# Optimization experiments

Hardware: AMD Instinct MI355X
Metric: run time of the kernel (lower is better)

The kernel has to match this reference:

```python
import jax, jax.numpy as jnp
import numpy as np

CAPACITY_FACTOR = 1.25


def setup_inputs() -> dict:
    key = jax.random.key(0)
    k1, k2, k3, k4, k5, k6 = jax.random.split(key, 6)
    N, d, E, h = 8192, 1024, 8, 2816
    x = jax.random.normal(k1, (N, d), dtype=jnp.float32)
    topK_indices = jax.random.randint(k2, (N,), 0, E, dtype=jnp.int64)
    topK_scores = jax.random.uniform(k3, (N,), dtype=jnp.float32)
    Wg = jax.random.normal(k4, (E, d, h), dtype=jnp.float32) * 0.02
    Wu = jax.random.normal(k5, (E, d, h), dtype=jnp.float32) * 0.02
    Wd = jax.random.normal(k6, (E, h, d), dtype=jnp.float32) * 0.02
    return {"x": x, "topK_indices": topK_indices, "topK_scores": topK_scores,
            "Wg": Wg, "Wu": Wu, "Wd": Wd}


def reference(x, topK_indices, topK_scores, Wg, Wu, Wd):
    # x: [N, d] tokens; topK_indices: [N] top-1 expert ids; per-expert SwiGLU FFN.
    N, d = x.shape
    E = Wg.shape[0]
    capacity = int(CAPACITY_FACTOR * N / E)  # = 1280

    idx = topK_indices.astype(jnp.int32)
    onehot = jax.nn.one_hot(idx, E, dtype=jnp.int32)            # [N, E]
    # position of each token within its expert's queue (first-come-first-served)
    pos = jnp.sum((jnp.cumsum(onehot, axis=0) - 1) * onehot, axis=1)  # [N]
    kept = pos < capacity                                        # dropped tokens pass through

    # flat dispatch slot: expert*capacity + pos for kept tokens, overflow bucket otherwise
    slots = jnp.where(kept, idx * capacity + pos, E * capacity)  # [N]
    buf = jnp.zeros((E * capacity + 1, d), dtype=x.dtype).at[slots].set(x)
    xe = buf[: E * capacity].reshape(E, capacity, d)             # [E, C, d]

    # per-expert SwiGLU FFN (grouped GEMMs)
    hgate = jnp.einsum('ecd,edh->ech', xe, Wg)
    hup = jnp.einsum('ecd,edh->ech', xe, Wu)
    hact = jax.nn.silu(hgate) * hup
    out = jnp.einsum('ech,ehd->ecd', hact, Wd).reshape(E * capacity, d)
    out = jnp.concatenate([out, jnp.zeros((1, d), out.dtype)], axis=0)

    y_tok = out[slots]                                           # gather back per token
    # multiply_gate_scores=True: scale expert output by routing score; dropped -> identity
    y = jnp.where(kept[:, None], y_tok * topK_scores[:, None], x)
    return y
```

## Files before the change

kernel.cpp:

```cpp
#include <hip/hip_runtime.h>
#include <cstdint>
#include <cstddef>

#define N_TOK 8192
#define DIM   1024
#define NEXP  8
#define HID   2816
#define CAP   1280

typedef __bf16 bf16x8 __attribute__((ext_vector_type(8)));
typedef float  floatx4 __attribute__((ext_vector_type(4)));

__device__ __forceinline__ unsigned short f2bf(float f) {
  return __builtin_bit_cast(unsigned short, (__bf16)f);
}
__device__ __forceinline__ float bf2f(unsigned short u) {
  return (float)__builtin_bit_cast(__bf16, u);
}

__device__ __forceinline__ void async16(void* lds, const void* g) {
  __builtin_amdgcn_global_load_lds(
      (const __attribute__((address_space(1))) void*)g,
      (__attribute__((address_space(3))) void*)lds, 16, 0, 0);
}

__global__ void route_kernel(const int* __restrict__ idx, int idx_stride,
                             int* __restrict__ slot,
                             int* __restrict__ slot_token,
                             int* __restrict__ counts) {
  __shared__ int hist[256][NEXP];
  const int t = threadIdx.x;
  int loc[NEXP];
#pragma unroll
  for (int e = 0; e < NEXP; e++) loc[e] = 0;
  const int base = t * 32;
  for (int i = 0; i < 32; i++) {
    int e = idx[(base + i) * idx_stride];
    loc[e]++;
  }
#pragma unroll
  for (int e = 0; e < NEXP; e++) hist[t][e] = loc[e];
  __syncthreads();
  if (t < NEXP) {
    int run = 0;
    for (int i = 0; i < 256; i++) { int v = hist[i][t]; hist[i][t] = run; run += v; }
    counts[t] = run < CAP ? run : CAP;
  }
  __syncthreads();
  int b2[NEXP];
#pragma unroll
  for (int e = 0; e < NEXP; e++) b2[e] = hist[t][e];
  for (int i = 0; i < 32; i++) {
    const int n = base + i;
    const int e = idx[n * idx_stride];
    const int p = b2[e]++;
    if (p < CAP) {
      const int s = e * CAP + p;
      slot[n] = s;
      slot_token[s] = n;
    } else {
      slot[n] = -1;
    }
  }
}

__global__ void dispatch_kernel(const float* __restrict__ x,
                                const int* __restrict__ slot,
                                unsigned short* __restrict__ xe,
                                float* __restrict__ y) {
  const int n = blockIdx.x;
  const int t = threadIdx.x;
  const int s = slot[n];
  const float4 v = ((const float4*)(x + (size_t)n * DIM))[t];
  if (s >= 0) {
    ushort4 b;
    b.x = f2bf(v.x); b.y = f2bf(v.y); b.z = f2bf(v.z); b.w = f2bf(v.w);
    ((ushort4*)(xe + (size_t)s * DIM))[t] = b;
  } else {
    ((float4*)(y + (size_t)n * DIM))[t] = v;
  }
}

__global__ void transpose_cvt(const float* __restrict__ in,
                              unsigned short* __restrict__ out,
                              const int R, const int C) {
  __shared__ float tile[32][33];
  const int e = blockIdx.z;
  const float* ib = in + (size_t)e * R * C;
  unsigned short* ob = out + (size_t)e * R * C;
  const int tx = threadIdx.x, ty = threadIdx.y;
  const int c0 = blockIdx.x * 32, r0 = blockIdx.y * 32;
#pragma unroll
  for (int i = 0; i < 4; i++)
    tile[ty + i * 8][tx] = ib[(size_t)(r0 + ty + i * 8) * C + c0 + tx];
  __syncthreads();
#pragma unroll
  for (int i = 0; i < 4; i++)
    ob[(size_t)(c0 + ty + i * 8) * R + r0 + tx] = f2bf(tile[tx][ty + i * 8]);
}

template <int EPI>
__global__ __launch_bounds__(256)
void moe_gemm(const unsigned short* __restrict__ A,
              const unsigned short* __restrict__ Bt,
              const int* __restrict__ counts,
              const int K, const int N,
              const size_t a_es, const size_t b_es,
              unsigned short* __restrict__ obuf,
              const int* __restrict__ slot_token,
              const float* __restrict__ scores,
              float* __restrict__ y) {
  const int e = blockIdx.z;
  const int cnt = counts[e];
  const int m0 = blockIdx.y * 128;
  if (m0 >= cnt) return;
  const int n0 = blockIdx.x * 128;

  __shared__ char smem[16384];

  const int t = threadIdx.x;
  const int lane = t & 63;
  const int w = t >> 6;
  const int wr = w >> 1;
  const int wc = w & 1;

  const unsigned short* aP  = A + e * a_es + (size_t)(m0 + (t >> 2)) * K + (t & 3) * 8;
  const unsigned short* bP  = Bt + e * b_es + (size_t)(n0 + (t >> 2)) * K + (t & 3) * 8;
  const unsigned short* aP1 = aP + (size_t)64 * K;
  const unsigned short* bP1 = bP + (size_t)64 * K;
  char* lA0 = smem + t * 16;
  char* lA1 = smem + 4096 + t * 16;
  char* lB0 = smem + 8192 + t * 16;
  char* lB1 = smem + 12288 + t * 16;

  floatx4 acc[4][4] = {};

  const int mrow = wr * 64 + (lane & 15);
  const int ncol = wc * 64 + (lane & 15);
  const int kq = (lane >> 4) * 16;

  for (int kk = 0; kk < K; kk += 32) {
    async16(lA0, aP); async16(lA1, aP1);
    async16(lB0, bP); async16(lB1, bP1);
    aP += 32; aP1 += 32; bP += 32; bP1 += 32;
    __syncthreads();
    bf16x8 af[4], bfr[4];
#pragma unroll
    for (int i = 0; i < 4; i++)
      af[i] = *(const bf16x8*)(smem + (mrow + i * 16) * 64 + kq);
#pragma unroll
    for (int i = 0; i < 4; i++)
      bfr[i] = *(const bf16x8*)(smem + 8192 + (ncol + i * 16) * 64 + kq);
#pragma unroll
    for (int mi = 0; mi < 4; mi++)
#pragma unroll
      for (int ni = 0; ni < 4; ni++)
        acc[mi][ni] = __builtin_amdgcn_mfma_f32_16x16x32_bf16(
            af[mi], bfr[ni], acc[mi][ni], 0, 0, 0);
    __syncthreads();
  }

  const int quad = lane >> 4;
  const int cl = lane & 15;

  if (EPI == 0) {
    unsigned short* ob = obuf + (size_t)e * CAP * N;
#pragma unroll
    for (int mi = 0; mi < 4; mi++)
#pragma unroll
      for (int r = 0; r < 4; r++) {
        const int row = m0 + wr * 64 + mi * 16 + quad * 4 + r;
        const size_t rb = (size_t)row * N;
#pragma unroll
        for (int ni = 0; ni < 4; ni++) {
          const int col = n0 + wc * 64 + ni * 16 + cl;
          ob[rb + col] = f2bf(acc[mi][ni][r]);
        }
      }
  } else if (EPI == 1) {
    unsigned short* ob = obuf + (size_t)e * CAP * N;
#pragma unroll
    for (int mi = 0; mi < 4; mi++)
#pragma unroll
      for (int r = 0; r < 4; r++) {
        const int row = m0 + wr * 64 + mi * 16 + quad * 4 + r;
        const size_t rb = (size_t)row * N;
#pragma unroll
        for (int ni = 0; ni < 4; ni++) {
          const int col = n0 + wc * 64 + ni * 16 + cl;
          const float g = bf2f(ob[rb + col]);
          const float u = acc[mi][ni][r];
          const float act = g / (1.0f + __expf(-g)) * u;
          ob[rb + col] = f2bf(act);
        }
      }
  } else {
#pragma unroll
    for (int mi = 0; mi < 4; mi++)
#pragma unroll
      for (int r = 0; r < 4; r++) {
        const int row = m0 + wr * 64 + mi * 16 + quad * 4 + r;
        if (row < cnt) {
          const int tok = slot_token[e * CAP + row];
          const float s = scores[tok];
          float* yr = y + (size_t)tok * DIM;
#pragma unroll
          for (int ni = 0; ni < 4; ni++) {
            const int col = n0 + wc * 64 + ni * 16 + cl;
            yr[col] = acc[mi][ni][r] * s;
          }
        }
      }
  }
}

extern "C" void kernel_launch(void* const* d_in, const int* in_sizes, int n_in,
                              void* d_out, int out_size, void* d_ws, size_t ws_size,
                              hipStream_t stream) {
  const float* x      = (const float*)d_in[0];
  const int*   idx    = (const int*)d_in[1];
  const float* scores = (const float*)d_in[2];
  const float* Wg     = (const float*)d_in[3];
  const float* Wu     = (const float*)d_in[4];
  const float* Wd     = (const float*)d_in[5];
  float* y = (float*)d_out;

  const int idx_stride = (in_sizes[1] == 2 * N_TOK) ? 2 : 1;

  char* ws = (char*)d_ws;
  size_t off = 0;
  auto alloc = [&](size_t b) -> char* {
    char* p = ws + off;
    off += (b + 255) & ~(size_t)255;
    return p;
  };
  int* counts            = (int*)alloc(NEXP * 4);
  int* slot              = (int*)alloc((size_t)N_TOK * 4);
  int* slot_token        = (int*)alloc((size_t)NEXP * CAP * 4);
  unsigned short* xe     = (unsigned short*)alloc((size_t)NEXP * CAP * DIM * 2);
  unsigned short* hbuf   = (unsigned short*)alloc((size_t)NEXP * CAP * HID * 2);
  unsigned short* wg_t   = (unsigned short*)alloc((size_t)NEXP * DIM * HID * 2);
  unsigned short* wu_t   = (unsigned short*)alloc((size_t)NEXP * DIM * HID * 2);
  unsigned short* wd_t   = (unsigned short*)alloc((size_t)NEXP * DIM * HID * 2);
  (void)ws_size; (void)n_in; (void)out_size;

  route_kernel<<<1, 256, 0, stream>>>(idx, idx_stride, slot, slot_token, counts);
  dispatch_kernel<<<N_TOK, 256, 0, stream>>>(x, slot, xe, y);

  dim3 tb(32, 8);
  transpose_cvt<<<dim3(HID / 32, DIM / 32, NEXP), tb, 0, stream>>>(Wg, wg_t, DIM, HID);
  transpose_cvt<<<dim3(HID / 32, DIM / 32, NEXP), tb, 0, stream>>>(Wu, wu_t, DIM, HID);
  transpose_cvt<<<dim3(DIM / 32, HID / 32, NEXP), tb, 0, stream>>>(Wd, wd_t, HID, DIM);

  moe_gemm<0><<<dim3(HID / 128, CAP / 128, NEXP), 256, 0, stream>>>(
      xe, wg_t, counts, DIM, HID, (size_t)CAP * DIM, (size_t)DIM * HID,
      hbuf, nullptr, nullptr, nullptr);
  moe_gemm<1><<<dim3(HID / 128, CAP / 128, NEXP), 256, 0, stream>>>(
      xe, wu_t, counts, DIM, HID, (size_t)CAP * DIM, (size_t)DIM * HID,
      hbuf, nullptr, nullptr, nullptr);
  moe_gemm<2><<<dim3(DIM / 128, CAP / 128, NEXP), 256, 0, stream>>>(
      hbuf, wd_t, counts, HID, DIM, (size_t)CAP * HID, (size_t)HID * DIM,
      nullptr, slot_token, scores, y);
}
```

Measured before the change: 645.0 us.

## Fuse gate/up GEMMs with SiLU epilogue, swizzle LDS, remap blocks per XCD

Gate and up projections now run in one kernel that shares the A tile and computes SiLU·up in registers. This removes the bf16 round trip of the gate output through global memory and one full pass over xe. LDS reads are XOR-swizzled to reduce bank conflicts. Blocks are remapped so each XCD works on contiguous expert/column groups, which should improve L2 reuse. The weight transpose uses 64x64 tiles with vectorized float4 loads and 16-byte stores.

```diff
diff --git a/kernel.cpp b/kernel.cpp
--- a/kernel.cpp
+++ b/kernel.cpp
@@ -10,12 +10,10 @@
 
 typedef __bf16 bf16x8 __attribute__((ext_vector_type(8)));
 typedef float  floatx4 __attribute__((ext_vector_type(4)));
+typedef unsigned short u16x8 __attribute__((ext_vector_type(8)));
 
 __device__ __forceinline__ unsigned short f2bf(float f) {
   return __builtin_bit_cast(unsigned short, (__bf16)f);
-}
-__device__ __forceinline__ float bf2f(unsigned short u) {
-  return (float)__builtin_bit_cast(__bf16, u);
 }
 
 __device__ __forceinline__ void async16(void* lds, const void* g) {
@@ -81,40 +79,58 @@
   }
 }
 
-__global__ void transpose_cvt(const float* __restrict__ in,
-                              unsigned short* __restrict__ out,
-                              const int R, const int C) {
-  __shared__ float tile[32][33];
+__global__ __launch_bounds__(256)
+void transpose_cvt(const float* __restrict__ in,
+                   unsigned short* __restrict__ out,
+                   const int R, const int C) {
+  __shared__ float tile[64][65];
   const int e = blockIdx.z;
   const float* ib = in + (size_t)e * R * C;
   unsigned short* ob = out + (size_t)e * R * C;
-  const int tx = threadIdx.x, ty = threadIdx.y;
-  const int c0 = blockIdx.x * 32, r0 = blockIdx.y * 32;
-#pragma unroll
-  for (int i = 0; i < 4; i++)
-    tile[ty + i * 8][tx] = ib[(size_t)(r0 + ty + i * 8) * C + c0 + tx];
+  const int t = threadIdx.x;
+  const int c0 = blockIdx.x * 64, r0 = blockIdx.y * 64;
+  const int lr = t >> 4;
+  const int lc = (t & 15) * 4;
+#pragma unroll
+  for (int i = 0; i < 4; i++) {
+    const float4 v = *(const float4*)(ib + (size_t)(r0 + lr + i * 16) * C + c0 + lc);
+    tile[lr + i * 16][lc + 0] = v.x;
+    tile[lr + i * 16][lc + 1] = v.y;
+    tile[lr + i * 16][lc + 2] = v.z;
+    tile[lr + i * 16][lc + 3] = v.w;
+  }
   __syncthreads();
-#pragma unroll
-  for (int i = 0; i < 4; i++)
-    ob[(size_t)(c0 + ty + i * 8) * R + r0 + tx] = f2bf(tile[tx][ty + i * 8]);
-}
-
-template <int EPI>
+  const int oc = t >> 2;
+  const int sub = t & 3;
+#pragma unroll
+  for (int half = 0; half < 2; half++) {
+    const int rch = sub + half * 4;
+    u16x8 o;
+#pragma unroll
+    for (int j = 0; j < 8; j++) o[j] = f2bf(tile[rch * 8 + j][oc]);
+    *(u16x8*)(ob + (size_t)(c0 + oc) * R + r0 + rch * 8) = o;
+  }
+}
+
 __global__ __launch_bounds__(256)
-void moe_gemm(const unsigned short* __restrict__ A,
-              const unsigned short* __restrict__ Bt,
-              const int* __restrict__ counts,
-              const int K, const int N,
-              const size_t a_es, const size_t b_es,
-              unsigned short* __restrict__ obuf,
-              const int* __restrict__ slot_token,
-              const float* __restrict__ scores,
-              float* __restrict__ y) {
-  const int e = blockIdx.z;
+void gateup_gemm(const unsigned short* __restrict__ A,
+                 const unsigned short* __restrict__ Bg,
+                 const unsigned short* __restrict__ Bu,
+                 const int* __restrict__ counts,
+                 unsigned short* __restrict__ hact) {
+  const int bid = blockIdx.x;
+  const int xcd = bid & 7;
+  const int slot = bid >> 3;
+  const int m = slot % 10;
+  const int cgl = slot / 10;
+  const int cg = xcd + 8 * cgl;
+  const int n = cg % 44;
+  const int e = cg / 44;
+
   const int cnt = counts[e];
-  const int m0 = blockIdx.y * 128;
+  const int m0 = m * 128;
   if (m0 >= cnt) return;
-  const int n0 = blockIdx.x * 128;
+  const int n0 = n * 64;
 
   __shared__ char smem[16384];
 
@@ -124,10 +140,106 @@
   const int wr = w >> 1;
   const int wc = w & 1;
 
-  const unsigned short* aP  = A + e * a_es + (size_t)(m0 + (t >> 2)) * K + (t & 3) * 8;
-  const unsigned short* bP  = Bt + e * b_es + (size_t)(n0 + (t >> 2)) * K + (t & 3) * 8;
-  const unsigned short* aP1 = aP + (size_t)64 * K;
-  const unsigned short* bP1 = bP + (size_t)64 * K;
+  const int sr = t >> 2;
+  const int sc = (t & 3) ^ ((sr >> 1) & 3);
+  const unsigned short* aP  = A  + (size_t)e * CAP * DIM + (size_t)(m0 + sr) * DIM + sc * 8;
+  const unsigned short* aP1 = aP + (size_t)64 * DIM;
+  const unsigned short* bgP = Bg + (size_t)e * HID * DIM + (size_t)(n0 + sr) * DIM + sc * 8;
+  const unsigned short* buP = Bu + (size_t)e * HID * DIM + (size_t)(n0 + sr) * DIM + sc * 8;
+  char* lA0 = smem + t * 16;
+  char* lA1 = smem + 4096 + t * 16;
+  char* lBg = smem + 8192 + t * 16;
+  char* lBu = smem + 12288 + t * 16;
+
+  floatx4 accg[4][2] = {};
+  floatx4 accu[4][2] = {};
+
+  const int mrow = wr * 64 + (lane & 15);
+  const int ncol = wc * 32 + (lane & 15);
+  const int q = lane >> 4;
+  const int kqA = ((q ^ ((mrow >> 1) & 3)) * 16);
+  const int kqB = ((q ^ ((ncol >> 1) & 3)) * 16);
+
+  for (int kk = 0; kk < DIM; kk += 32) {
+    async16(lA0, aP); async16(lA1, aP1);
+    async16(lBg, bgP); async16(lBu, buP);
+    aP += 32; aP1 += 32; bgP += 32; buP += 32;
+    __syncthreads();
+    bf16x8 af[4], gf[2], uf[2];
+#pragma unroll
+    for (int i = 0; i < 4; i++)
+      af[i] = *(const bf16x8*)(smem + (mrow + i * 16) * 64 + kqA);
+#pragma unroll
+    for (int i = 0; i < 2; i++) {
+      gf[i] = *(const bf16x8*)(smem + 8192 + (ncol + i * 16) * 64 + kqB);
+      uf[i] = *(const bf16x8*)(smem + 12288 + (ncol + i * 16) * 64 + kqB);
+    }
+#pragma unroll
+    for (int mi = 0; mi < 4; mi++)
+#pragma unroll
+      for (int ni = 0; ni < 2; ni++) {
+        accg[mi][ni] = __builtin_amdgcn_mfma_f32_16x16x32_bf16(
+            af[mi], gf[ni], accg[mi][ni], 0, 0, 0);
+        accu[mi][ni] = __builtin_amdgcn_mfma_f32_16x16x32_bf16(
+            af[mi], uf[ni], accu[mi][ni], 0, 0, 0);
+      }
+    __syncthreads();
+  }
+
+  const int quad = lane >> 4;
+  const int cl = lane & 15;
+  unsigned short* ob = hact + (size_t)e * CAP * HID;
+#pragma unroll
+  for (int mi = 0; mi < 4; mi++)
+#pragma unroll
+    for (int r = 0; r < 4; r++) {
+      const int row = m0 + wr * 64 + mi * 16 + quad * 4 + r;
+      const size_t rb = (size_t)row * HID;
+#pragma unroll
+      for (int ni = 0; ni < 2; ni++) {
+        const int col = n0 + wc * 32 + ni * 16 + cl;
+        const float g = accg[mi][ni][r];
+        const float u = accu[mi][ni][r];
+        ob[rb + col] = f2bf(g / (1.0f + __expf(-g)) * u);
+      }
+    }
+}
+
+__global__ __launch_bounds__(256)
+void down_gemm(const unsigned short* __restrict__ A,
+               const unsigned short* __restrict__ Bt,
+               const int* __restrict__ counts,
+               const int* __restrict__ slot_token,
+               const float* __restrict__ scores,
+               float* __restrict__ y) {
+  const int bid = blockIdx.x;
+  const int xcd = bid & 7;
+  const int slot = bid >> 3;
+  const int m = slot % 10;
+  const int cgl = slot / 10;
+  const int cg = xcd + 8 * cgl;
+  const int n = cg % 8;
+  const int e = cg / 8;
+
+  const int cnt = counts[e];
+  const int m0 = m * 128;
+  if (m0 >= cnt) return;
+  const int n0 = n * 128;
+
+  __shared__ char smem[16384];
+
+  const int t = threadIdx.x;
+  const int lane = t & 63;
+  const int w = t >> 6;
+  const int wr = w >> 1;
+  const int wc = w & 1;
+
+  const int sr = t >> 2;
+  const int sc = (t & 3) ^ ((sr >> 1) & 3);
+  const unsigned short* aP  = A + (size_t)e * CAP * HID + (size_t)(m0 + sr) * HID + sc * 8;
+  const unsigned short* aP1 = aP + (size_t)64 * HID;
+  const unsigned short* bP  = Bt + (size_t)e * DIM * HID + (size_t)(n0 + sr) * HID + sc * 8;
+  const unsigned short* bP1 = bP + (size_t)64 * HID;
   char* lA0 = smem + t * 16;
   char* lA1 = smem + 4096 + t * 16;
   char* lB0 = smem + 8192 + t * 16;
@@ -137,9 +249,11 @@
 
   const int mrow = wr * 64 + (lane & 15);
   const int ncol = wc * 64 + (lane & 15);
-  const int kq = (lane >> 4) * 16;
-
-  for (int kk = 0; kk < K; kk += 32) {
+  const int q = lane >> 4;
+  const int kqA = ((q ^ ((mrow >> 1) & 3)) * 16);
+  const int kqB = ((q ^ ((ncol >> 1) & 3)) * 16);
+
+  for (int kk = 0; kk < HID; kk += 32) {
     async16(lA0, aP); async16(lA1, aP1);
     async16(lB0, bP); async16(lB1, bP1);
     aP += 32; aP1 += 32; bP += 32; bP1 += 32;
@@ -147,10 +261,10 @@
     bf16x8 af[4], bfr[4];
 #pragma unroll
     for (int i = 0; i < 4; i++)
-      af[i] = *(const bf16x8*)(smem + (mrow + i * 16) * 64 + kq);
+      af[i] = *(const bf16x8*)(smem + (mrow + i * 16) * 64 + kqA);
 #pragma unroll
     for (int i = 0; i < 4; i++)
-      bfr[i] = *(const bf16x8*)(smem + 8192 + (ncol + i * 16) * 64 + kq);
+      bfr[i] = *(const bf16x8*)(smem + 8192 + (ncol + i * 16) * 64 + kqB);
 #pragma unroll
     for (int mi = 0; mi < 4; mi++)
 #pragma unroll
@@ -162,56 +276,22 @@
 
   const int quad = lane >> 4;
   const int cl = lane & 15;
-
-  if (EPI == 0) {
-    unsigned short* ob = obuf + (size_t)e * CAP * N;
-#pragma unroll
-    for (int mi = 0; mi < 4; mi++)
-#pragma unroll
-      for (int r = 0; r < 4; r++) {
-        const int row = m0 + wr * 64 + mi * 16 + quad * 4 + r;
-        const size_t rb = (size_t)row * N;
+#pragma unroll
+  for (int mi = 0; mi < 4; mi++)
+#pragma unroll
+    for (int r = 0; r < 4; r++) {
+      const int row = m0 + wr * 64 + mi * 16 + quad * 4 + r;
+      if (row < cnt) {
+        const int tok = slot_token[e * CAP + row];
+        const float s = scores[tok];
+        float* yr = y + (size_t)tok * DIM;
 #pragma unroll
         for (int ni = 0; ni < 4; ni++) {
           const int col = n0 + wc * 64 + ni * 16 + cl;
-          ob[rb + col] = f2bf(acc[mi][ni][r]);
+          yr[col] = acc[mi][ni][r] * s;
         }
       }
-  } else if (EPI == 1) {
-    unsigned short* ob = obuf + (size_t)e * CAP * N;
-#pragma unroll
-    for (int mi = 0; mi < 4; mi++)
-#pragma unroll
-      for (int r = 0; r < 4; r++) {
-        const int row = m0 + wr * 64 + mi * 16 + quad * 4 + r;
-        const size_t rb = (size_t)row * N;
-#pragma unroll
-        for (int ni = 0; ni < 4; ni++) {
-          const int col = n0 + wc * 64 + ni * 16 + cl;
-          const float g = bf2f(ob[rb + col]);
-          const float u = acc[mi][ni][r];
-          const float act = g / (1.0f + __expf(-g)) * u;
-          ob[rb + col] = f2bf(act);
-        }
-      }
-  } else {
-#pragma unroll
-    for (int mi = 0; mi < 4; mi++)
-#pragma unroll
-      for (int r = 0; r < 4; r++) {
-        const int row = m0 + wr * 64 + mi * 16 + quad * 4 + r;
-        if (row < cnt) {
-          const int tok = slot_token[e * CAP + row];
-          const float s = scores[tok];
-          float* yr = y + (size_t)tok * DIM;
-#pragma unroll
-          for (int ni = 0; ni < 4; ni++) {
-            const int col = n0 + wc * 64 + ni * 16 + cl;
-            yr[col] = acc[mi][ni][r] * s;
-          }
-        }
-      }
-  }
+    }
 }
 
 extern "C" void kernel_launch(void* const* d_in, const int* in_sizes, int n_in,
@@ -238,7 +318,7 @@
   int* slot              = (int*)alloc((size_t)N_TOK * 4);
   int* slot_token        = (int*)alloc((size_t)NEXP * CAP * 4);
   unsigned short* xe     = (unsigned short*)alloc((size_t)NEXP * CAP * DIM * 2);
-  unsigned short* hbuf   = (unsigned short*)alloc((size_t)NEXP * CAP * HID * 2);
+  unsigned short* hact   = (unsigned short*)alloc((size_t)NEXP * CAP * HID * 2);
   unsigned short* wg_t   = (unsigned short*)alloc((size_t)NEXP * DIM * HID * 2);
   unsigned short* wu_t   = (unsigned short*)alloc((size_t)NEXP * DIM * HID * 2);
   unsigned short* wd_t   = (unsigned short*)alloc((size_t)NEXP * DIM * HID * 2);
@@ -247,18 +327,10 @@
   route_kernel<<<1, 256, 0, stream>>>(idx, idx_stride, slot, slot_token, counts);
   dispatch_kernel<<<N_TOK, 256, 0, stream>>>(x, slot, xe, y);
 
-  dim3 tb(32, 8);
-  transpose_cvt<<<dim3(HID / 32, DIM / 32, NEXP), tb, 0, stream>>>(Wg, wg_t, DIM, HID);
-  transpose_cvt<<<dim3(HID / 32, DIM / 32, NEXP), tb, 0, stream>>>(Wu, wu_t, DIM, HID);
-  transpose_cvt<<<dim3(DIM / 32, HID / 32, NEXP), tb, 0, stream>>>(Wd, wd_t, HID, DIM);
-
-  moe_gemm<0><<<dim3(HID / 128, CAP / 128, NEXP), 256, 0, stream>>>(
-      xe, wg_t, counts, DIM, HID, (size_t)CAP * DIM, (size_t)DIM * HID,
-      hbuf, nullptr, nullptr, nullptr);
-  moe_gemm<1><<<dim3(HID / 128, CAP / 128, NEXP), 256, 0, stream>>>(
-      xe, wu_t, counts, DIM, HID, (size_t)CAP * DIM, (size_t)DIM * HID,
-      hbuf, nullptr, nullptr, nullptr);
-  moe_gemm<2><<<dim3(DIM / 128, CAP / 128, NEXP), 256, 0, stream>>>(
-      hbuf, wd_t, counts, HID, DIM, (size_t)CAP * HID, (size_t)HID * DIM,
-      nullptr, slot_token, scores, y);
-}
+  transpose_cvt<<<dim3(HID / 64, DIM / 64, NEXP), 256, 0, stream>>>(Wg, wg_t, DIM, HID);
+  transpose_cvt<<<dim3(HID / 64, DIM / 64, NEXP), 256, 0, stream>>>(Wu, wu_t, DIM, HID);
+  transpose_cvt<<<dim3(DIM / 64, HID / 64, NEXP), 256, 0, stream>>>(Wd, wd_t, HID, DIM);
+
+  gateup_gemm<<<8 * 44 * 10, 256, 0, stream>>>(xe, wg_t, wu_t, counts, hact);
+  down_gemm<<<8 * 8 * 10, 256, 0, stream>>>(hact, wd_t, counts, slot_token, scores, y);
+}
```

Result: faster. 560.9 us (-13.0%).
